# Kernel tuning notes

Hardware: AMD Instinct MI355X
Metric: run time of the kernel (lower is better)

The kernel has to match this reference:

```python
import jax, jax.numpy as jnp
import numpy as np

N = 4096
DEG = 16.0
KC = 64  # max closed-neighborhood size supported (deg~16 graph => safe)


def setup_inputs() -> dict:
    key = jax.random.key(0)
    ks = jax.random.split(key, 6)
    u = jax.random.uniform(ks[0], (N, N))
    upper = jnp.triu((u < (DEG / N)).astype(jnp.float32), k=1)
    adj = upper + upper.T  # symmetric 0/1, zero diagonal
    d = 64
    return {
        'adj': adj,
        'e_w': jax.random.normal(ks[1], (15, d), dtype=jnp.float32) * 0.25,
        'e_b': jnp.zeros((d,), jnp.float32),
        'w1': jax.random.normal(ks[2], (3, d, d), dtype=jnp.float32) * 0.125,
        'b1': jnp.zeros((3, d), jnp.float32),
        'w2': jax.random.normal(ks[3], (3, d, d), dtype=jnp.float32) * 0.125,
        'b2': jnp.zeros((3, d), jnp.float32),
        'eps': jnp.zeros((3,), jnp.float32),
    }


def cr_feat(adj):
    n = adj.shape[0]
    m = adj + jnp.eye(n, dtype=adj.dtype)  # closed-neighborhood indicator rows [N,N]
    k = m.sum(1)                            # |S_v|
    D = m @ adj                             # D[v,u] = degree of u inside S_v (A symmetric)
    E = 0.5 * jnp.sum(m * D, axis=1)        # edges inside S_v
    W = jnp.sum(m * D * (D - 1.0) * 0.5, axis=1)  # wedges inside S_v
    vals, idx = jax.lax.top_k(m, KC)        # members of S_v (padded)
    valid = (vals > 0.5).astype(adj.dtype)
    sub = adj[idx[:, :, None], idx[:, None, :]]        # [N,KC,KC] induced subgraph
    sub = sub * valid[:, :, None] * valid[:, None, :]
    T = jnp.einsum('vij,vjk,vki->v', sub, sub, sub) / 6.0  # triangles inside S_v
    f3 = T
    f2 = W - 3.0 * T
    f1 = E * (k - 2.0) - 2.0 * f2 - 3.0 * f3
    tot = k * (k - 1.0) * (k - 2.0) / 6.0   # C(k,3) = total triples
    f0 = tot - f1 - f2 - f3
    f = jnp.stack([f0, f1, f2, f3], axis=1)
    f = jnp.where((k >= 3.0)[:, None], f, 0.0)  # original skips |nb|<3
    return f / (jnp.sum(f, axis=1, keepdims=True) + 1e-10)


def ww_feat(adj):
    a2 = adj @ adj
    a4 = a2 @ a2                             # matrix_power(adj, 4)
    vals, _ = jax.lax.top_k(a4, 8)           # per-row sort desc, top 8
    return vals


def degree_feat(adj):
    d = adj.sum(1)
    diag_a2 = jnp.einsum('vu,uv->v', adj, adj)  # diag(A@A)
    return jnp.stack([d, d ** 2, diag_a2], axis=1)


def _forward(adj, e_w, e_b, w1, b1, w2, b2, eps):
    feats = jnp.concatenate([cr_feat(adj), ww_feat(adj), degree_feat(adj)], axis=1)  # [N,15]
    x = feats @ e_w + e_b
    for i in range(3):
        h = (1.0 + eps[i]) * x + adj @ x
        x = jax.nn.relu(h @ w1[i] + b1[i]) @ w2[i] + b2[i]
    return x.sum(0)


def reference(adj, e_w, e_b, w1, b1, w2, b2, eps):
    return _forward(adj, e_w, e_b, w1, b1, w2, b2, eps)
```

## Files before the change

### kernel.cpp

```cpp
#include <hip/hip_runtime.h>
#include <hip/hip_bf16.h>
#include <stdint.h>

#define NN 4096


__global__ __launch_bounds__(256) void scan_k(const float* __restrict__ adj,
                                              int* __restrict__ nbr,
                                              int* __restrict__ deg,
                                              unsigned long long* __restrict__ abits,
                                              float* __restrict__ feats) {
    __shared__ int nlist[4][64];
    int tid = threadIdx.x;
    int wv = tid >> 6, ln = tid & 63;
    int v = blockIdx.x * 4 + wv;
    size_t rb = (size_t)v * NN;
    int total = 0;
    unsigned long long w0 = 0;
    const float4* row4 = (const float4*)(adj + rb);
    for (int base = 0; base < NN; base += 256) {
        float4 f = row4[(base >> 2) + ln];
        int q4 = (base >> 8) << 2;
        #pragma unroll
        for (int j = 0; j < 4; j++) {
            float vj = (j == 0) ? f.x : (j == 1) ? f.y : (j == 2) ? f.z : f.w;
            unsigned long long m = __ballot(vj > 0.5f);
            if (vj > 0.5f) {
                int pos = total + __popcll(m & ((1ull << ln) - 1ull));
                if (pos < 64) nlist[wv][pos] = base + 4 * ln + j;
            }
            if (ln == q4 + j) w0 = m;
            total += __popcll(m);
        }
    }
    abits[(size_t)v * 64 + ln] = w0;
    int degL = min(total, 64);
    if (ln < degL) nbr[v * 64 + ln] = nlist[wv][ln];
    if (ln == 0) {
        deg[v] = total;
        float degf = (float)total;
        feats[v * 16 + 12] = degf;
        feats[v * 16 + 13] = degf * degf;
        feats[v * 16 + 14] = degf;
    }
}

__global__ __launch_bounds__(256) void cra2_k(const unsigned long long* __restrict__ abits,
                                              const int* __restrict__ nbr,
                                              const int* __restrict__ deg,
                                              unsigned int* __restrict__ a3d,
                                              float* __restrict__ feats) {
    __shared__ __align__(64) unsigned int smem[NN + 132 + 640];
    int tid = threadIdx.x;
    int bid = blockIdx.x;
    int wv = tid >> 6, ln = tid & 63;

    if (bid < NN) {
        unsigned int* acc   = smem;
        int* us             = (int*)(smem + NN);
        int* dus            = (int*)(smem + NN + 64);
        unsigned int* wsumS = smem + NN + 128;
        unsigned int* srcL  = smem + NN + 132;
        int v = bid;
        uint4 z = {0u, 0u, 0u, 0u};
        #pragma unroll
        for (int i = 0; i < 4; i++) ((uint4*)acc)[tid + 256 * i] = z;
        int dv = min(deg[v], 64);
        if (tid < dv) {
            int u = nbr[v * 64 + tid];
            us[tid] = u;
            dus[tid] = min(deg[u], 64);
        }
        __syncthreads();
        for (int p = tid; p < dv * 64; p += 256) {
            int i = p >> 6, wi = p & 63;
            if (wi < dus[i]) atomicAdd(&acc[nbr[us[i] * 64 + wi]], 1u);
        }
        __syncthreads();
        unsigned int myw[16];
        int local = 0;
        #pragma unroll
        for (int m = 0; m < 16; m++) {
            unsigned int a = acc[tid + 256 * m];
            myw[m] = a;
            local += (a != 0u);
        }
        int incl = local;
        #pragma unroll
        for (int off = 1; off < 64; off <<= 1) {
            int n = __shfl_up(incl, off, 64);
            if (ln >= off) incl += n;
        }
        if (ln == 63) wsumS[wv] = (unsigned int)incl;
        __syncthreads();
        unsigned int wpre = 0, nsrc = 0;
        #pragma unroll
        for (int q = 0; q < 4; q++) {
            unsigned int s = wsumS[q];
            if (q < wv) wpre += s;
            nsrc += s;
        }
        unsigned int pos = wpre + (unsigned int)(incl - local);
        #pragma unroll
        for (int m = 0; m < 16; m++) {
            unsigned int a = myw[m];
            if (a) {
                unsigned int col = (unsigned int)tid + 256u * m;
                unsigned int dgu = (unsigned int)min(deg[col], 64);
                if (pos < 640u) srcL[pos] = (a << 19) | (dgu << 12) | col;
                pos++;
            }
        }
        if (nsrc > 640u) nsrc = 640u;
        __syncthreads();
        #pragma unroll
        for (int i = 0; i < 4; i++) ((uint4*)acc)[tid + 256 * i] = z;
        __syncthreads();
        int lim64 = (((int)nsrc + 1) >> 1) << 6;
        for (int q = tid; q < lim64; q += 256) {
            int s = (q >> 5) & ~0;
            s = ((q >> 6) << 1) | ((q >> 5) & 1);
            int j = q & 31;
            if (s < (int)nsrc) {
                unsigned int e = srcL[s];
                int dgu = (int)((e >> 12) & 0x7Fu);
                unsigned int w = e >> 19;
                const int* nru = nbr + (e & 0xFFFu) * 64;
                if (j < dgu) atomicAdd(&acc[nru[j]], w);
                if (j == 31) {
                    for (int jj = 32; jj < dgu; jj++) atomicAdd(&acc[nru[jj]], w);
                }
            }
        }
        __syncthreads();
        {
            int base = tid * 16;
            unsigned int w0 = 0, w1 = 0, w2 = 0, w3 = 0;
            #pragma unroll
            for (int i = 0; i < 4; i++) w0 |= min(acc[base + i], 255u) << (8 * i);
            #pragma unroll
            for (int i = 0; i < 4; i++) w1 |= min(acc[base + 4 + i], 255u) << (8 * i);
            #pragma unroll
            for (int i = 0; i < 4; i++) w2 |= min(acc[base + 8 + i], 255u) << (8 * i);
            #pragma unroll
            for (int i = 0; i < 4; i++) w3 |= min(acc[base + 12 + i], 255u) << (8 * i);
            uint4 o; o.x = w0; o.y = w1; o.z = w2; o.w = w3;
            ((uint4*)((char*)a3d + (size_t)v * 4096))[tid] = o;
        }
    } else {
        unsigned long long* rows = (unsigned long long*)smem;
        int* mems = (int*)(smem + 1024);
        int v = (bid - NN) * 4 + wv;

        int dv = deg[v];
        int degL = min(dv, 64);
        int c = min(dv + 1, 64);

        int nl = (ln < degL) ? nbr[v * 64 + ln] : 0;
        int isless = (ln < degL && nl < v) ? 1 : 0;
        int pos = isless;
        #pragma unroll
        for (int off = 32; off; off >>= 1) pos += __shfl_xor(pos, off, 64);

        int mem = 0;
        if (ln < c) {
            if (ln < pos)       mem = nl;
            else if (ln == pos) mem = v;
            else                mem = nbr[v * 64 + ln - 1];
        }
        mems[wv * 64 + ln] = mem;
        __syncthreads();

        unsigned long long mask = 0ull;
        {
            const unsigned long long* rowb = abits + (size_t)mem * 64;
            for (int j = 0; j < c; j++) {
                int mj = mems[wv * 64 + j];
                unsigned long long w = rowb[((mj >> 8) << 2) | (mj & 3)];
                mask |= ((w >> ((mj >> 2) & 63)) & 1ull) << j;
            }
        }
        if (ln >= c) mask = 0ull;
        rows[wv * 64 + ln] = mask;
        __syncthreads();

        int tpart = 0;
        float epart = 0.f, wpart = 0.f;
        if (ln < c) {
            unsigned long long mm = mask;
            while (mm) {
                int j = __ffsll(mm) - 1;
                mm &= mm - 1;
                tpart += __popcll(mask & rows[wv * 64 + j]);
            }
            if (ln != pos) {
                int cn = __popcll(rows[wv * 64 + pos] & mask);
                float D2 = (float)cn + 1.0f;
                epart = D2;
                wpart = D2 * (D2 - 1.0f) * 0.5f;
            }
        }
        float es = epart, wsum2 = wpart;
        int ts = tpart;
        #pragma unroll
        for (int off = 32; off; off >>= 1) {
            es += __shfl_xor(es, off, 64);
            wsum2 += __shfl_xor(wsum2, off, 64);
            ts += __shfl_xor(ts, off, 64);
        }

        if (ln == 0) {
            float degf = (float)dv;
            float k = degf + 1.0f;
            float E = 0.5f * (es + degf);
            float W = wsum2 + degf * (degf - 1.0f) * 0.5f;
            float T = (float)ts / 6.0f;
            float f3 = T;
            float f2 = W - 3.0f * T;
            float f1 = E * (k - 2.0f) - 2.0f * f2 - 3.0f * f3;
            float tot2 = k * (k - 1.0f) * (k - 2.0f) / 6.0f;
            float f0 = tot2 - f1 - f2 - f3;
            if (k < 3.0f) { f0 = f1 = f2 = f3 = 0.f; }
            float s = f0 + f1 + f2 + f3 + 1e-10f;
            feats[v * 16 + 0] = f0 / s;
            feats[v * 16 + 1] = f1 / s;
            feats[v * 16 + 2] = f2 / s;
            feats[v * 16 + 3] = f3 / s;
        }
    }
}

__global__ __launch_bounds__(1024) void order_k(const int* __restrict__ deg,
                                                int* __restrict__ ord) {
    __shared__ unsigned int bcnt[192];
    __shared__ unsigned int bbase[192];
    int tid = threadIdx.x;
    if (tid < 192) bcnt[tid] = 0u;
    __syncthreads();
    unsigned char myk[4];
    #pragma unroll
    for (int j = 0; j < 4; j++) {
        int v = tid * 4 + j;
        myk[j] = (unsigned char)min(deg[v], 191);
        atomicAdd(&bcnt[myk[j]], 1u);
    }
    __syncthreads();
    if (tid == 0) {
        unsigned int run = 0;
        for (int b = 191; b >= 0; b--) { bbase[b] = run; run += bcnt[b]; }
    }
    __syncthreads();
    #pragma unroll
    for (int j = 0; j < 4; j++) {
        int v = tid * 4 + j;
        unsigned int p = atomicAdd(&bbase[myk[j]], 1u);
        ord[p] = v;
    }
}

#define DOPAIRS(word, jb) \
    { unsigned int p0 = ((word) & 0xFFu) | (((word) & 0xFF00u) << 8);       \
      unsigned int p1 = (((word) >> 16) & 0xFFu) | (((word) >> 24) << 16);  \
      atomicAdd(&acc[a1e ^ (jb + 0u)], p0);                                 \
      atomicAdd(&acc[a1e ^ (jb + 1u)], p1); }

__global__ __launch_bounds__(512) void a4row_k(const uint4* __restrict__ a3d4,
                                               const int* __restrict__ deg,
                                               const int* __restrict__ nbr,
                                               const int* __restrict__ ord,
                                               const float* __restrict__ feats,
                                               const float* __restrict__ e_w,
                                               const float* __restrict__ e_b,
                                               float* __restrict__ x0) {
    __shared__ __align__(64) unsigned int acc[NN / 2];
    __shared__ unsigned int sbase[64];
    __shared__ unsigned int wtops[64];
    int tid = threadIdx.x;
    int wv = tid >> 6, ln = tid & 63;
    int v = ord[blockIdx.x];

    {
        uint4 z = {0u, 0u, 0u, 0u};
        ((uint4*)acc)[tid] = z;
    }
    int dvv = min(deg[v], 64);
    if (tid < dvv) sbase[tid] = (unsigned int)nbr[v * 64 + tid] * 256u;
    __syncthreads();

    int tot = dvv << 8;
    for (int g = tid; g < tot; g += 512) {
        unsigned int d = (unsigned int)g & 255u;
        uint4 E = a3d4[sbase[g >> 8] + d];
        unsigned int a1e = (d << 3) | ((d >> 2) & 7u);
        DOPAIRS(E.x, 0u)
        DOPAIRS(E.y, 2u)
        DOPAIRS(E.z, 4u)
        DOPAIRS(E.w, 6u)
    }
    __syncthreads();

    unsigned int best[8];
    #pragma unroll
    for (int q = 0; q < 8; q++) best[q] = 0u;
    #pragma unroll
    for (int m = 0; m < 4; m++) {
        unsigned int w = acc[tid + 512 * m];
        #pragma unroll
        for (int hlf = 0; hlf < 2; hlf++) {
            unsigned int val = hlf ? (w >> 16) : (w & 0xFFFFu);
            if (val > best[7]) {
                best[7] = val;
                #pragma unroll
                for (int s = 7; s > 0; s--) {
                    if (best[s] > best[s - 1]) {
                        unsigned int t2 = best[s - 1]; best[s - 1] = best[s]; best[s] = t2;
                    } else break;
                }
            }
        }
    }

    unsigned int wave_val = 0u;
    #pragma unroll
    for (int r = 0; r < 8; r++) {
        unsigned int m = best[0];
        #pragma unroll
        for (int off = 32; off; off >>= 1)
            m = max(m, (unsigned int)__shfl_xor((int)m, off, 64));
        unsigned long long bb = __ballot(best[0] == m);
        int src = __ffsll(bb) - 1;
        if (ln == src) {
            #pragma unroll
            for (int s = 0; s < 7; s++) best[s] = best[s + 1];
            best[7] = 0u;
        }
        if (ln == r) wave_val = m;
    }
    if (ln < 8) wtops[wv * 8 + ln] = wave_val;
    __syncthreads();

    if (wv == 0) {
        unsigned int cand = wtops[ln];
        unsigned int myv = 0u;
        #pragma unroll
        for (int r = 0; r < 8; r++) {
            unsigned int m = cand;
            #pragma unroll
            for (int off = 32; off; off >>= 1)
                m = max(m, (unsigned int)__shfl_xor((int)m, off, 64));
            unsigned long long bb = __ballot(cand == m);
            int src = __ffsll(bb) - 1;
            if (ln == src) cand = 0u;
            if (ln == r) myv = m;
        }
        int d = ln;
        float s = e_b[d];
        s += feats[v * 16 + 0]  * e_w[0 * 64 + d];
        s += feats[v * 16 + 1]  * e_w[1 * 64 + d];
        s += feats[v * 16 + 2]  * e_w[2 * 64 + d];
        s += feats[v * 16 + 3]  * e_w[3 * 64 + d];
        #pragma unroll
        for (int j = 0; j < 8; j++) {
            float mj = (float)(unsigned int)__shfl((int)myv, j, 64);
            s += mj * e_w[(4 + j) * 64 + d];
        }
        s += feats[v * 16 + 12] * e_w[12 * 64 + d];
        s += feats[v * 16 + 13] * e_w[13 * 64 + d];
        s += feats[v * 16 + 14] * e_w[14 * 64 + d];
        x0[(size_t)v * 64 + d] = s;
    }
}

__global__ __launch_bounds__(256) void layer_k(const float* __restrict__ xin,
                                               float* __restrict__ xout,
                                               const float* __restrict__ w1,
                                               const float* __restrict__ b1,
                                               const float* __restrict__ w2,
                                               const float* __restrict__ b2,
                                               const float* __restrict__ eps,
                                               const int* __restrict__ nbr,
                                               const int* __restrict__ deg,
                                               float* __restrict__ out,
                                               int li) {
    __shared__ float wL[4096];
    __shared__ float h[4][64], t[4][64];
    int tid = threadIdx.x;
    int wv = tid >> 6, d = tid & 63;
    int v = blockIdx.x * 4 + wv;

    {
        const float4* src = (const float4*)(w1 + li * 4096);
        #pragma unroll
        for (int i = 0; i < 4; i++) ((float4*)wL)[tid + 256 * i] = src[tid + 256 * i];
    }

    float xv = xin[(size_t)v * 64 + d];
    int dv = min(deg[v], 64);
    const int* nl = nbr + v * 64;
    float agg = 0.f;
    int j = 0;
    for (; j + 4 <= dv; j += 4) {
        int n0 = nl[j], n1 = nl[j + 1], n2 = nl[j + 2], n3 = nl[j + 3];
        float a0 = xin[(size_t)n0 * 64 + d];
        float a1 = xin[(size_t)n1 * 64 + d];
        float a2v = xin[(size_t)n2 * 64 + d];
        float a3 = xin[(size_t)n3 * 64 + d];
        agg += (a0 + a1) + (a2v + a3);
    }
    for (; j < dv; j++) agg += xin[(size_t)nl[j] * 64 + d];
    float hv = (1.0f + eps[li]) * xv + agg;
    h[wv][d] = hv;
    __syncthreads();

    float s = b1[li * 64 + d];
    #pragma unroll 8
    for (int k = 0; k < 64; k++) s += h[wv][k] * wL[k * 64 + d];
    s = fmaxf(s, 0.f);
    t[wv][d] = s;
    __syncthreads();

    {
        const float4* src = (const float4*)(w2 + li * 4096);
        #pragma unroll
        for (int i = 0; i < 4; i++) ((float4*)wL)[tid + 256 * i] = src[tid + 256 * i];
    }
    __syncthreads();

    float o = b2[li * 64 + d];
    #pragma unroll 8
    for (int k = 0; k < 64; k++) o += t[wv][k] * wL[k * 64 + d];
    if (li == 2) {
        h[wv][d] = o;
        __syncthreads();
        if (wv == 0)
            atomicAdd(&out[d], (h[0][d] + h[1][d]) + (h[2][d] + h[3][d]));
    } else {
        xout[(size_t)v * 64 + d] = o;
    }
}

extern "C" void kernel_launch(void* const* d_in, const int* in_sizes, int n_in,
                              void* d_out, int out_size, void* d_ws, size_t ws_size,
                              hipStream_t stream) {
    const float* adj = (const float*)d_in[0];
    const float* e_w = (const float*)d_in[1];
    const float* e_b = (const float*)d_in[2];
    const float* w1  = (const float*)d_in[3];
    const float* b1  = (const float*)d_in[4];
    const float* w2  = (const float*)d_in[5];
    const float* b2  = (const float*)d_in[6];
    const float* eps = (const float*)d_in[7];
    float* out = (float*)d_out;

    char* ws = (char*)d_ws;
    unsigned int*       a3d     = (unsigned int*)(ws);
    int*                nbr     = (int*)(ws + 25165824);
    int*                deg     = (int*)(ws + 26214400);
    float*              feats   = (float*)(ws + 26247168);
    float*              x0      = (float*)(ws + 26509312);
    float*              x1      = (float*)(ws + 27557888);
    unsigned long long* abits   = (unsigned long long*)(ws + 28868608);
    int*                ord     = (int*)(ws + 30969856);

    hipMemsetAsync(out, 0, 64 * sizeof(float), stream);
    scan_k<<<1024, 256, 0, stream>>>(adj, nbr, deg, abits, feats);
    cra2_k<<<5120, 256, 0, stream>>>(abits, nbr, deg, a3d, feats);
    order_k<<<1, 1024, 0, stream>>>(deg, ord);
    a4row_k<<<4096, 512, 0, stream>>>((const uint4*)a3d, deg, nbr, ord, feats, e_w, e_b, x0);
    layer_k<<<1024, 256, 0, stream>>>(x0, x1, w1, b1, w2, b2, eps, nbr, deg, out, 0);
    layer_k<<<1024, 256, 0, stream>>>(x1, x0, w1, b1, w2, b2, eps, nbr, deg, out, 1);
    layer_k<<<1024, 256, 0, stream>>>(x0, x1, w1, b1, w2, b2, eps, nbr, deg, out, 2);
}
```

Before: 265.3 us.

## Store A^3 rows as 4-bit nibbles with sparse overflow side list

The intermediate A^3 rows are stored as 4-bit saturated nibbles instead of 8-bit bytes, with entries above 15 written to a per-row side list of (excess, column) pairs plus a count. The A^4 row kernel now reads half as many bytes per neighbour row, unpacks nibbles with byte-permute instructions into packed 16-bit accumulators, then adds the side-list corrections. This halves the main memory traffic for the A^3 gather, at the cost of a prefix scan in the producer, an extra sparse atomic pass, and silent truncation if a row has more than 192 overflow entries.

```diff
diff --git a/kernel.cpp b/kernel.cpp
--- a/kernel.cpp
+++ b/kernel.cpp
@@ -48,7 +48,9 @@
 __global__ __launch_bounds__(256) void cra2_k(const unsigned long long* __restrict__ abits,
                                               const int* __restrict__ nbr,
                                               const int* __restrict__ deg,
-                                              unsigned int* __restrict__ a3d,
+                                              unsigned int* __restrict__ a3n,
+                                              unsigned int* __restrict__ side,
+                                              unsigned int* __restrict__ scnt,
                                               float* __restrict__ feats) {
     __shared__ __align__(64) unsigned int smem[NN + 132 + 640];
     int tid = threadIdx.x;
@@ -118,8 +120,7 @@
         __syncthreads();
         int lim64 = (((int)nsrc + 1) >> 1) << 6;
         for (int q = tid; q < lim64; q += 256) {
-            int s = (q >> 5) & ~0;
-            s = ((q >> 6) << 1) | ((q >> 5) & 1);
+            int s = ((q >> 6) << 1) | ((q >> 5) & 1);
             int j = q & 31;
             if (s < (int)nsrc) {
                 unsigned int e = srcL[s];
@@ -133,20 +134,51 @@
             }
         }
         __syncthreads();
+        unsigned int wAn = 0, wBn = 0, ovm = 0;
+        #pragma unroll
+        for (int i2 = 0; i2 < 8; i2++) {
+            unsigned int a = acc[8 * tid + i2];
+            wAn |= min(a, 15u) << (4 * i2);
+            ovm |= (a > 15u ? 1u : 0u) << i2;
+        }
+        #pragma unroll
+        for (int i2 = 0; i2 < 8; i2++) {
+            unsigned int a = acc[2048 + 8 * tid + i2];
+            wBn |= min(a, 15u) << (4 * i2);
+            ovm |= (a > 15u ? 1u : 0u) << (8 + i2);
+        }
         {
-            int base = tid * 16;
-            unsigned int w0 = 0, w1 = 0, w2 = 0, w3 = 0;
-            #pragma unroll
-            for (int i = 0; i < 4; i++) w0 |= min(acc[base + i], 255u) << (8 * i);
-            #pragma unroll
-            for (int i = 0; i < 4; i++) w1 |= min(acc[base + 4 + i], 255u) << (8 * i);
-            #pragma unroll
-            for (int i = 0; i < 4; i++) w2 |= min(acc[base + 8 + i], 255u) << (8 * i);
-            #pragma unroll
-            for (int i = 0; i < 4; i++) w3 |= min(acc[base + 12 + i], 255u) << (8 * i);
-            uint4 o; o.x = w0; o.y = w1; o.z = w2; o.w = w3;
-            ((uint4*)((char*)a3d + (size_t)v * 4096))[tid] = o;
-        }
+            uint2 nw; nw.x = wAn; nw.y = wBn;
+            ((uint2*)((char*)a3n + (size_t)v * 2048))[tid] = nw;
+        }
+        int lov = __popc(ovm);
+        int inc2 = lov;
+        #pragma unroll
+        for (int off = 1; off < 64; off <<= 1) {
+            int n = __shfl_up(inc2, off, 64);
+            if (ln >= off) inc2 += n;
+        }
+        if (ln == 63) wsumS[wv] = (unsigned int)inc2;
+        __syncthreads();
+        unsigned int wpre2 = 0, totS = 0;
+        #pragma unroll
+        for (int q = 0; q < 4; q++) {
+            unsigned int s = wsumS[q];
+            if (q < wv) wpre2 += s;
+            totS += s;
+        }
+        unsigned int pos2 = wpre2 + (unsigned int)(inc2 - lov);
+        unsigned int* sideR = side + (size_t)v * 192;
+        while (ovm) {
+            int i2 = __ffs(ovm) - 1;
+            ovm &= ovm - 1;
+            unsigned int col = (i2 < 8) ? (unsigned int)(8 * tid + i2)
+                                        : (unsigned int)(2048 + 8 * tid + (i2 - 8));
+            unsigned int a = acc[col];
+            if (pos2 < 192u) sideR[pos2] = ((a - 15u) << 16) | col;
+            pos2++;
+        }
+        if (tid == 0) scnt[v] = min(totS, 192u);
     } else {
         unsigned long long* rows = (unsigned long long*)smem;
         int* mems = (int*)(smem + 1024);
@@ -258,13 +290,17 @@
     }
 }
 
-#define DOPAIRS(word, jb) \
-    { unsigned int p0 = ((word) & 0xFFu) | (((word) & 0xFF00u) << 8);       \
-      unsigned int p1 = (((word) >> 16) & 0xFFu) | (((word) >> 24) << 16);  \
-      atomicAdd(&acc[a1e ^ (jb + 0u)], p0);                                 \
-      atomicAdd(&acc[a1e ^ (jb + 1u)], p1); }
-
-__global__ __launch_bounds__(512) void a4row_k(const uint4* __restrict__ a3d4,
+#define DONIB(w, a1e) \
+    { unsigned int x_ = (w) & 0x0F0F0F0Fu;                                      \
+      unsigned int y_ = ((w) >> 4) & 0x0F0F0F0Fu;                               \
+      atomicAdd(&acc[(a1e) ^ 0u], __builtin_amdgcn_perm(y_, x_, 0x0c040c00u));  \
+      atomicAdd(&acc[(a1e) ^ 1u], __builtin_amdgcn_perm(y_, x_, 0x0c050c01u));  \
+      atomicAdd(&acc[(a1e) ^ 2u], __builtin_amdgcn_perm(y_, x_, 0x0c060c02u));  \
+      atomicAdd(&acc[(a1e) ^ 3u], __builtin_amdgcn_perm(y_, x_, 0x0c070c03u)); }
+
+__global__ __launch_bounds__(512) void a4row_k(const uint2* __restrict__ a3n2,
+                                               const unsigned int* __restrict__ side,
+                                               const unsigned int* __restrict__ scnt,
                                                const int* __restrict__ deg,
                                                const int* __restrict__ nbr,
                                                const int* __restrict__ ord,
@@ -274,6 +310,7 @@
                                                float* __restrict__ x0) {
     __shared__ __align__(64) unsigned int acc[NN / 2];
     __shared__ unsigned int sbase[64];
+    __shared__ unsigned int sS[64];
     __shared__ unsigned int wtops[64];
     int tid = threadIdx.x;
     int wv = tid >> 6, ln = tid & 63;
@@ -284,18 +321,32 @@
         ((uint4*)acc)[tid] = z;
     }
     int dvv = min(deg[v], 64);
-    if (tid < dvv) sbase[tid] = (unsigned int)nbr[v * 64 + tid] * 256u;
-    __syncthreads();
-
-    int tot = dvv << 8;
-    for (int g = tid; g < tot; g += 512) {
-        unsigned int d = (unsigned int)g & 255u;
-        uint4 E = a3d4[sbase[g >> 8] + d];
-        unsigned int a1e = (d << 3) | ((d >> 2) & 7u);
-        DOPAIRS(E.x, 0u)
-        DOPAIRS(E.y, 2u)
-        DOPAIRS(E.z, 4u)
-        DOPAIRS(E.w, 6u)
+    if (tid < dvv) {
+        unsigned int u = (unsigned int)nbr[v * 64 + tid];
+        sbase[tid] = u;
+        sS[tid] = scnt[u];
+    }
+    __syncthreads();
+
+    int tot1 = dvv << 8;
+    for (int g = tid; g < tot1; g += 512) {
+        unsigned int q = (unsigned int)g & 255u;
+        uint2 W = a3n2[sbase[g >> 8] * 256u + q];
+        unsigned int a1e = (q << 2) | ((q >> 3) & 3u);
+        DONIB(W.x, a1e)
+        DONIB(W.y, a1e + 1024u)
+    }
+    for (int i = wv; i < dvv; i += 8) {
+        int ns = (int)sS[i];
+        const unsigned int* sp = side + (size_t)sbase[i] * 192;
+        for (int g2 = ln; g2 < ns; g2 += 64) {
+            unsigned int e = sp[g2];
+            unsigned int col = e & 0xFFFu;
+            unsigned int w = e >> 16;
+            unsigned int pidx = col >> 1;
+            unsigned int ad = pidx ^ ((pidx >> 5) & 3u);
+            atomicAdd(&acc[ad], w << ((col & 1u) << 4));
+        }
     }
     __syncthreads();
 
@@ -453,7 +504,9 @@
     float* out = (float*)d_out;
 
     char* ws = (char*)d_ws;
-    unsigned int*       a3d     = (unsigned int*)(ws);
+    unsigned int*       a3n     = (unsigned int*)(ws);
+    unsigned int*       side    = (unsigned int*)(ws + 8388608);
+    unsigned int*       scnt    = (unsigned int*)(ws + 11534336);
     int*                nbr     = (int*)(ws + 25165824);
     int*                deg     = (int*)(ws + 26214400);
     float*              feats   = (float*)(ws + 26247168);
@@ -464,9 +517,9 @@
 
     hipMemsetAsync(out, 0, 64 * sizeof(float), stream);
     scan_k<<<1024, 256, 0, stream>>>(adj, nbr, deg, abits, feats);
-    cra2_k<<<5120, 256, 0, stream>>>(abits, nbr, deg, a3d, feats);
+    cra2_k<<<5120, 256, 0, stream>>>(abits, nbr, deg, a3n, side, scnt, feats);
     order_k<<<1, 1024, 0, stream>>>(deg, ord);
-    a4row_k<<<4096, 512, 0, stream>>>((const uint4*)a3d, deg, nbr, ord, feats, e_w, e_b, x0);
+    a4row_k<<<4096, 512, 0, stream>>>((const uint2*)a3n, side, scnt, deg, nbr, ord, feats, e_w, e_b, x0);
     layer_k<<<1024, 256, 0, stream>>>(x0, x1, w1, b1, w2, b2, eps, nbr, deg, out, 0);
     layer_k<<<1024, 256, 0, stream>>>(x1, x0, w1, b1, w2, b2, eps, nbr, deg, out, 1);
     layer_k<<<1024, 256, 0, stream>>>(x0, x1, w1, b1, w2, b2, eps, nbr, deg, out, 2);
```

Measured after the change: 262.6 us. Within noise of the previous version (-1.0%).
